# Performance work log

Hardware: AMD Instinct MI355X
Metric: run time of the kernel (lower is better)

## Reference

```python
import jax, jax.numpy as jnp
import numpy as np

N_NODES = 50000
N_EDGES = 800000
IN, HID, OUT = 512, 256, 128


def spmm(edge_src, edge_dst, edge_weight, x, n_nodes):
    # y[i] = sum_{e: dst[e]==i} w[e] * x[src[e]]   (sparse adjacency @ x)
    msgs = edge_weight[:, None] * x[edge_src]          # [E, F] gather
    return jax.ops.segment_sum(msgs, edge_dst, num_segments=n_nodes)


def setup_inputs() -> dict:
    key = jax.random.key(0)
    k1, k2, k3, k4, k5, k6 = jax.random.split(key, 6)
    features = jax.random.normal(k1, (N_NODES, IN), dtype=jnp.float32)
    edge_src = jax.random.randint(k2, (N_EDGES,), 0, N_NODES, dtype=jnp.int32)
    edge_dst = jax.random.randint(k3, (N_EDGES,), 0, N_NODES, dtype=jnp.int32)
    edge_weight = jax.random.uniform(k4, (N_EDGES,), dtype=jnp.float32)
    # init like torch: uniform(-stdv, stdv), stdv = 1/sqrt(out_dim)
    s1 = 1.0 / np.sqrt(HID)
    s2 = 1.0 / np.sqrt(OUT)
    W1 = jax.random.uniform(k5, (IN, HID), dtype=jnp.float32, minval=-s1, maxval=s1)
    W2 = jax.random.uniform(k6, (HID, OUT), dtype=jnp.float32, minval=-s2, maxval=s2)
    return {"features": features, "edge_src": edge_src, "edge_dst": edge_dst,
            "edge_weight": edge_weight, "W1": W1, "W2": W2}


def reference(features, edge_src, edge_dst, edge_weight, W1, W2):
    n = features.shape[0]
    # layer 1: dense GEMM -> SpMM -> ReLU
    hidden = jax.nn.relu(spmm(edge_src, edge_dst, edge_weight, features @ W1, n))
    # layer 2: dense GEMM -> SpMM
    out = spmm(edge_src, edge_dst, edge_weight, hidden @ W2, n)
    return out
```

## Files before the change

kernel.cpp:

```cpp
#include <hip/hip_runtime.h>

#define NN 50000
#define NE 800000
#define FIN 512
#define FHID 256
#define FOUT 128
#define MPAD 50048

#define TW1_BLOCKS  512
#define TW2_BLOCKS  128
#define ZERO_BLOCKS 13

#define NBKT   196
#define BCAP   5120
#define BSTRIDE 16
#define PA_BLOCKS 392
#define E_CHA    2048

#define PB_BLOCKS    196
#define GEMM1_BLOCKS 1564
#define GEMM2_BLOCKS 782

using bf16x8 = __attribute__((ext_vector_type(8))) short;
using f32x4  = __attribute__((ext_vector_type(4))) float;
using u16x8  = __attribute__((ext_vector_type(8))) unsigned short;
using u16x4  = __attribute__((ext_vector_type(4))) unsigned short;

__device__ __forceinline__ unsigned short f2bf(float f) {
    unsigned int u = __builtin_bit_cast(unsigned int, f);
    unsigned int r = (u + 0x7FFFu + ((u >> 16) & 1u)) >> 16;
    return (unsigned short)r;
}
__device__ __forceinline__ float bf2f(unsigned short u) {
    return __builtin_bit_cast(float, (unsigned int)u << 16);
}
__device__ __forceinline__ void gload_lds16(const void* g, void* l) {
    __builtin_amdgcn_global_load_lds(
        (const __attribute__((address_space(1))) void*)g,
        (__attribute__((address_space(3))) void*)l, 16, 0, 0);
}


__global__ __launch_bounds__(256) void prep_kernel(
    int* __restrict__ bcur,
    const float* __restrict__ W1, unsigned short* __restrict__ W1T,
    const float* __restrict__ W2, unsigned short* __restrict__ W2T) {
    int b = blockIdx.x, tid = threadIdx.x;
    if (b < TW1_BLOCKS) {
        int t = b * 256 + tid;
        int n = t % FHID, k = t / FHID;
        W1T[(size_t)n * FIN + k] = f2bf(W1[t]);
    } else if (b < TW1_BLOCKS + TW2_BLOCKS) {
        int t = (b - TW1_BLOCKS) * 256 + tid;
        int n = t % FOUT, k = t / FOUT;
        W2T[(size_t)n * FHID + k] = f2bf(W2[t]);
    } else {
        int i = (b - TW1_BLOCKS - TW2_BLOCKS) * 256 + tid;
        if (i < NBKT * BSTRIDE) bcur[i] = 0;
    }
}


__device__ __forceinline__ void passa_body(int pa,
                                           const int* __restrict__ src,
                                           const int* __restrict__ dst,
                                           const float* __restrict__ w,
                                           int* __restrict__ bcur,
                                           int2* __restrict__ barr) {
    __shared__ int hist[NBKT];
    __shared__ int resv[NBKT];
    int tid = threadIdx.x;
    if (tid < NBKT) hist[tid] = 0;
    __syncthreads();
    int base = pa * E_CHA + tid;
    int  d[8];
    bool m[8];
#pragma unroll
    for (int j = 0; j < 8; ++j) {
        int e = base + j * 256;
        m[j] = e < NE;
        d[j] = m[j] ? dst[e] : 0;
    }
#pragma unroll
    for (int j = 0; j < 8; ++j)
        if (m[j]) atomicAdd(&hist[d[j] >> 8], 1);
    __syncthreads();
    if (tid < NBKT) {
        int h = hist[tid];
        resv[tid] = (h > 0) ? atomicAdd(&bcur[tid * BSTRIDE], h) : 0;
        hist[tid] = 0;
    }
    __syncthreads();
    int   s[8];
    float wv[8];
#pragma unroll
    for (int j = 0; j < 8; ++j) {
        int e = base + j * 256;
        s[j]  = m[j] ? src[e] : 0;
        wv[j] = m[j] ? w[e] : 0.f;
    }
#pragma unroll
    for (int j = 0; j < 8; ++j) {
        if (m[j]) {
            int bb = d[j] >> 8;
            int r  = atomicAdd(&hist[bb], 1);
            int pos = resv[bb] + r;
            if (pos < BCAP)
                barr[(size_t)bb * BCAP + pos] =
                    make_int2(s[j] | ((d[j] & 255) << 16), __float_as_int(wv[j]));
        }
    }
}


__device__ __forceinline__ void gemm1_body(const float* __restrict__ X,
                                           const unsigned short* __restrict__ BT,
                                           unsigned short* __restrict__ C,
                                           int bx, int by) {
    __shared__ unsigned short As[64 * 64];
    __shared__ unsigned short Bs[128 * 64];

    const int tid  = threadIdx.x;
    const int lane = tid & 63;
    const int wid  = tid >> 6;
    const int wm   = wid >> 1;
    const int wn   = wid & 1;
    const int brow = bx * 64;
    const int bcol = by * 128;
    const int r15   = lane & 15;
    const int khalf = (lane >> 4) * 8;

    f32x4 acc[2][4] = {};

    for (int k0 = 0; k0 < FIN; k0 += 64) {
#pragma unroll
        for (int c = 0; c < 4; ++c) {
            int b   = wid * 4096 + c * 1024 + lane * 16;
            int row = b >> 7;
            int cby = (b & 127) ^ ((row & 7) << 4);
            const char* gb = (const char*)(BT + (size_t)(bcol + row) * FIN + k0) + cby;
            gload_lds16(gb, (char*)Bs + wid * 4096 + c * 1024);
        }
#pragma unroll
        for (int g = 0; g < 2; ++g) {
            int idx  = g * 256 + tid;
            int row  = idx >> 3;
            int col0 = (idx & 7) * 8;
            float4 a0 = make_float4(0.f, 0.f, 0.f, 0.f), a1 = a0;
            int grow = brow + row;
            if (grow < NN) {
                const float4* p = (const float4*)(X + (size_t)grow * FIN + k0 + col0);
                a0 = p[0]; a1 = p[1];
            }
            u16x8 v;
            v[0] = f2bf(a0.x); v[1] = f2bf(a0.y); v[2] = f2bf(a0.z); v[3] = f2bf(a0.w);
            v[4] = f2bf(a1.x); v[5] = f2bf(a1.y); v[6] = f2bf(a1.z); v[7] = f2bf(a1.w);
            int byte = row * 128 + ((col0 * 2) ^ ((row & 7) << 4));
            *(u16x8*)((char*)As + byte) = v;
        }
        __syncthreads();

        bf16x8 af[2][2], bfr[4][2];
#pragma unroll
        for (int m = 0; m < 2; ++m) {
            int row = wm * 32 + m * 16 + r15;
            int rb  = row * 128;
            int sw  = (row & 7) << 4;
#pragma unroll
            for (int ks = 0; ks < 2; ++ks) {
                int byte = rb + (((ks * 32 + khalf) * 2) ^ sw);
                af[m][ks] = *(const bf16x8*)((const char*)As + byte);
            }
        }
#pragma unroll
        for (int n = 0; n < 4; ++n) {
            int row = wn * 64 + n * 16 + r15;
            int rb  = row * 128;
            int sw  = (row & 7) << 4;
#pragma unroll
            for (int ks = 0; ks < 2; ++ks) {
                int byte = rb + (((ks * 32 + khalf) * 2) ^ sw);
                bfr[n][ks] = *(const bf16x8*)((const char*)Bs + byte);
            }
        }
#pragma unroll
        for (int m = 0; m < 2; ++m)
#pragma unroll
            for (int n = 0; n < 4; ++n)
#pragma unroll
                for (int ks = 0; ks < 2; ++ks)
                    acc[m][n] = __builtin_amdgcn_mfma_f32_16x16x32_bf16(
                        af[m][ks], bfr[n][ks], acc[m][n], 0, 0, 0);
        __syncthreads();
    }

    const int crow0 = brow + wm * 32;
    const int ccol0 = bcol + wn * 64 + r15;
    const int rsub  = (lane >> 4) * 4;
#pragma unroll
    for (int m = 0; m < 2; ++m) {
#pragma unroll
        for (int r = 0; r < 4; ++r) {
            int grow = crow0 + m * 16 + rsub + r;
            if (grow < NN) {
#pragma unroll
                for (int n = 0; n < 4; ++n)
                    C[(size_t)grow * FHID + ccol0 + n * 16] = f2bf(acc[m][n][r]);
            }
        }
    }
}


__global__ __launch_bounds__(256) void fused_passa_gemm1_kernel(
    const int* __restrict__ src, const int* __restrict__ dst,
    const float* __restrict__ w, int* __restrict__ bcur, int2* __restrict__ barr,
    const float* __restrict__ X, const unsigned short* __restrict__ BT,
    unsigned short* __restrict__ C) {
    if (blockIdx.x < PA_BLOCKS) {
        passa_body(blockIdx.x, src, dst, w, bcur, barr);
    } else {
        int g = blockIdx.x - PA_BLOCKS;
        gemm1_body(X, BT, C, g >> 1, g & 1);
    }
}


__global__ __launch_bounds__(256) void passb_kernel(const int2* __restrict__ barr,
                                                    const int* __restrict__ bcur,
                                                    int* __restrict__ off,
                                                    int2* __restrict__ csr) {
    __shared__ int sc[256];
    __shared__ int cnt[256];
    __shared__ int pre[256];
    __shared__ int wsum[4];
    int b = blockIdx.x, tid = threadIdx.x, lane = tid & 63, wid = tid >> 6;

    int v = (tid < NBKT) ? min(bcur[tid * BSTRIDE], BCAP) : 0;
    int s = v;
#pragma unroll
    for (int d = 1; d < 64; d <<= 1) {
        int t = __shfl_up(s, d, 64);
        if (lane >= d) s += t;
    }
    if (lane == 63) wsum[wid] = s;
    __syncthreads();
    int wo = 0;
#pragma unroll
    for (int j = 0; j < 4; ++j)
        if (j < wid) wo += wsum[j];
    sc[tid] = wo + s - v;
    if (b == 0 && tid == NBKT - 1) off[NN] = wo + s;
    cnt[tid] = 0;
    __syncthreads();

    int bko_b = sc[b];
    int total = min(bcur[b * BSTRIDE], BCAP);
    const int2* seg = barr + (size_t)b * BCAP;

    for (int k = tid; k < total; k += 256)
        atomicAdd(&cnt[(seg[k].x >> 16) & 255], 1);
    __syncthreads();
    int v2 = cnt[tid];
    int s2 = v2;
#pragma unroll
    for (int d = 1; d < 64; d <<= 1) {
        int t = __shfl_up(s2, d, 64);
        if (lane >= d) s2 += t;
    }
    if (lane == 63) wsum[wid] = s2;
    __syncthreads();
    int wo2 = 0;
#pragma unroll
    for (int j = 0; j < 4; ++j)
        if (j < wid) wo2 += wsum[j];
    int base = bko_b + wo2 + s2 - v2;
    pre[tid] = base;
    int n = b * 256 + tid;
    if (n < NN) off[n] = base;
    cnt[tid] = 0;
    __syncthreads();
    for (int k = tid; k < total; k += 256) {
        int2 pl = seg[k];
        int dlow = (pl.x >> 16) & 255;
        int r = atomicAdd(&cnt[dlow], 1);
        csr[pre[dlow] + r] = make_int2(pl.x & 0xFFFF, pl.y);
    }
}


__global__ __launch_bounds__(256) void gemm2_kernel(const unsigned short* __restrict__ A,
                                                    const unsigned short* __restrict__ BT,
                                                    unsigned short* __restrict__ C) {
    __shared__ unsigned short As[64 * 64];
    __shared__ unsigned short Bs[128 * 64];

    const int tid  = threadIdx.x;
    const int lane = tid & 63;
    const int wid  = tid >> 6;
    const int wm   = wid >> 1;
    const int wn   = wid & 1;
    const int brow = blockIdx.x * 64;
    const int r15   = lane & 15;
    const int khalf = (lane >> 4) * 8;

    f32x4 acc[2][4] = {};

    for (int k0 = 0; k0 < FHID; k0 += 64) {
#pragma unroll
        for (int c = 0; c < 4; ++c) {
            int b   = wid * 4096 + c * 1024 + lane * 16;
            int row = b >> 7;
            int cby = (b & 127) ^ ((row & 7) << 4);
            const char* gb = (const char*)(BT + (size_t)row * FHID + k0) + cby;
            gload_lds16(gb, (char*)Bs + wid * 4096 + c * 1024);
        }
#pragma unroll
        for (int c = 0; c < 2; ++c) {
            int b   = wid * 2048 + c * 1024 + lane * 16;
            int row = b >> 7;
            int cby = (b & 127) ^ ((row & 7) << 4);
            const char* ga = (const char*)(A + (size_t)(brow + row) * FHID + k0) + cby;
            gload_lds16(ga, (char*)As + wid * 2048 + c * 1024);
        }
        __syncthreads();

        bf16x8 af[2][2], bfr[4][2];
#pragma unroll
        for (int m = 0; m < 2; ++m) {
            int row = wm * 32 + m * 16 + r15;
            int rb  = row * 128;
            int sw  = (row & 7) << 4;
#pragma unroll
            for (int ks = 0; ks < 2; ++ks) {
                int byte = rb + (((ks * 32 + khalf) * 2) ^ sw);
                af[m][ks] = *(const bf16x8*)((const char*)As + byte);
            }
        }
#pragma unroll
        for (int n = 0; n < 4; ++n) {
            int row = wn * 64 + n * 16 + r15;
            int rb  = row * 128;
            int sw  = (row & 7) << 4;
#pragma unroll
            for (int ks = 0; ks < 2; ++ks) {
                int byte = rb + (((ks * 32 + khalf) * 2) ^ sw);
                bfr[n][ks] = *(const bf16x8*)((const char*)Bs + byte);
            }
        }
#pragma unroll
        for (int m = 0; m < 2; ++m)
#pragma unroll
            for (int n = 0; n < 4; ++n)
#pragma unroll
                for (int ks = 0; ks < 2; ++ks)
                    acc[m][n] = __builtin_amdgcn_mfma_f32_16x16x32_bf16(
                        af[m][ks], bfr[n][ks], acc[m][n], 0, 0, 0);
        __syncthreads();
    }

    const int crow0 = brow + wm * 32;
    const int ccol0 = wn * 64 + r15;
    const int rsub  = (lane >> 4) * 4;
#pragma unroll
    for (int m = 0; m < 2; ++m) {
#pragma unroll
        for (int r = 0; r < 4; ++r) {
            int grow = crow0 + m * 16 + rsub + r;
            if (grow < NN) {
#pragma unroll
                for (int n = 0; n < 4; ++n)
                    C[(size_t)grow * FOUT + ccol0 + n * 16] = f2bf(acc[m][n][r]);
            }
        }
    }
}


__global__ __launch_bounds__(256) void spmm_pair_kernel(const unsigned short* __restrict__ X,
                                                        const int* __restrict__ off,
                                                        const int2* __restrict__ csr,
                                                        unsigned short* __restrict__ Y) {
    int wave = (int)((blockIdx.x * 256 + threadIdx.x) >> 6);
    int lane = threadIdx.x & 63;
    int half = lane >> 5;
    int hl   = lane & 31;
    int n = wave * 2 + half;
    if (n >= NN) return;
    int e0 = off[n];
    int e1 = off[n + 1];
    const size_t fo = (size_t)hl * 8;

    float acc[8] = {};
    for (int e = e0; e < e1; e += 8) {
        int   ss[8];
        float ww[8];
#pragma unroll
        for (int j = 0; j < 8; ++j) {
            int  ee = e + j;
            bool v  = ee < e1;
            int2 sw = csr[v ? ee : e0];
            ss[j] = sw.x;
            ww[j] = v ? __int_as_float(sw.y) : 0.f;
        }
        u16x8 r[8];
#pragma unroll
        for (int j = 0; j < 8; ++j)
            r[j] = *(const u16x8*)(X + (size_t)ss[j] * FHID + fo);
#pragma unroll
        for (int j = 0; j < 8; ++j)
#pragma unroll
            for (int k = 0; k < 8; ++k)
                acc[k] += ww[j] * bf2f(r[j][k]);
    }
    u16x8 o;
#pragma unroll
    for (int k = 0; k < 8; ++k) o[k] = f2bf(fmaxf(acc[k], 0.f));
    *(u16x8*)(Y + (size_t)n * FHID + fo) = o;
}


__global__ __launch_bounds__(256) void spmm_quad_kernel(const unsigned short* __restrict__ X,
                                                        const int* __restrict__ off,
                                                        const int2* __restrict__ csr,
                                                        float* __restrict__ Y) {
    int wave = (int)((blockIdx.x * 256 + threadIdx.x) >> 6);
    int lane = threadIdx.x & 63;
    int q  = lane >> 4;
    int hl = lane & 15;
    int n = wave * 4 + q;
    if (n >= NN) return;
    int e0 = off[n];
    int e1 = off[n + 1];
    const size_t fo = (size_t)hl * 8;

    float acc[8] = {};
    for (int e = e0; e < e1; e += 8) {
        int   ss[8];
        float ww[8];
#pragma unroll
        for (int j = 0; j < 8; ++j) {
            int  ee = e + j;
            bool v  = ee < e1;
            int2 sw = csr[v ? ee : e0];
            ss[j] = sw.x;
            ww[j] = v ? __int_as_float(sw.y) : 0.f;
        }
        u16x8 r[8];
#pragma unroll
        for (int j = 0; j < 8; ++j)
            r[j] = *(const u16x8*)(X + (size_t)ss[j] * FOUT + fo);
#pragma unroll
        for (int j = 0; j < 8; ++j)
#pragma unroll
            for (int k = 0; k < 8; ++k)
                acc[k] += ww[j] * bf2f(r[j][k]);
    }
    float4 o0 = make_float4(acc[0], acc[1], acc[2], acc[3]);
    float4 o1 = make_float4(acc[4], acc[5], acc[6], acc[7]);
    *(float4*)(Y + (size_t)n * FOUT + fo) = o0;
    *(float4*)(Y + (size_t)n * FOUT + fo + 4) = o1;
}


extern "C" void kernel_launch(void* const* d_in, const int* in_sizes, int n_in,
                              void* d_out, int out_size, void* d_ws, size_t ws_size,
                              hipStream_t stream) {
    const float* features = (const float*)d_in[0];
    const int*   edge_src = (const int*)d_in[1];
    const int*   edge_dst = (const int*)d_in[2];
    const float* edge_w   = (const float*)d_in[3];
    const float* W1       = (const float*)d_in[4];
    const float* W2       = (const float*)d_in[5];
    float* out = (float*)d_out;

    char*  ws  = (char*)d_ws;
    size_t ofs = 0;
    auto carve = [&](size_t bytes) -> void* {
        void* r = ws + ofs;
        ofs = (ofs + bytes + 255) & ~(size_t)255;
        return r;
    };
    int*            off   = (int*)carve((NN + 1) * sizeof(int));
    int*            bcur  = (int*)carve(NBKT * BSTRIDE * sizeof(int));
    int2*           barr  = (int2*)carve((size_t)NBKT * BCAP * sizeof(int2));
    int2*           csr   = (int2*)carve((size_t)NE * sizeof(int2));
    unsigned short* W1T   = (unsigned short*)carve((size_t)FHID * FIN * 2);
    unsigned short* W2T   = (unsigned short*)carve((size_t)FOUT * FHID * 2);
    unsigned short* H0b   = (unsigned short*)carve((size_t)MPAD * FHID * 2);
    unsigned short* Hb    = (unsigned short*)carve((size_t)MPAD * FHID * 2);
    unsigned short* H1b   = H0b;

    prep_kernel<<<TW1_BLOCKS + TW2_BLOCKS + ZERO_BLOCKS, 256, 0, stream>>>(
        bcur, W1, W1T, W2, W2T);

    fused_passa_gemm1_kernel<<<PA_BLOCKS + GEMM1_BLOCKS, 256, 0, stream>>>(
        edge_src, edge_dst, edge_w, bcur, barr, features, W1T, H0b);

    passb_kernel<<<PB_BLOCKS, 256, 0, stream>>>(barr, bcur, off, csr);

    spmm_pair_kernel<<<6250, 256, 0, stream>>>(H0b, off, csr, Hb);

    gemm2_kernel<<<GEMM2_BLOCKS, 256, 0, stream>>>(Hb, W2T, H1b);
    spmm_quad_kernel<<<3125, 256, 0, stream>>>(H1b, off, csr, out);
}
```

Baseline: 168.2 us.

## Double-buffer LDS tiles in both GEMM kernels to overlap loads with MFMA

Both GEMM kernels now keep two LDS buffers for the A and B tiles. The next K-slice is fetched while MFMAs run on the current one: global_load_lds for B (and A in gemm2), and register prefetch plus a deferred bf16 convert-and-store for A in gemm1. This drops one barrier per iteration and hides global load latency behind compute. In exchange, LDS use per block doubles to 48KB, which may lower occupancy, and gemm1 keeps extra prefetch registers live.

Measured after the change: 169.5 us. No clear change (+0.8%).

```diff
diff --git a/kernel.cpp b/kernel.cpp
--- a/kernel.cpp
+++ b/kernel.cpp
@@ -24,7 +24,6 @@
 using bf16x8 = __attribute__((ext_vector_type(8))) short;
 using f32x4  = __attribute__((ext_vector_type(4))) float;
 using u16x8  = __attribute__((ext_vector_type(8))) unsigned short;
-using u16x4  = __attribute__((ext_vector_type(4))) unsigned short;
 
 __device__ __forceinline__ unsigned short f2bf(float f) {
     unsigned int u = __builtin_bit_cast(unsigned int, f);
@@ -117,8 +116,8 @@
                                            const unsigned short* __restrict__ BT,
                                            unsigned short* __restrict__ C,
                                            int bx, int by) {
-    __shared__ unsigned short As[64 * 64];
-    __shared__ unsigned short Bs[128 * 64];
+    __shared__ unsigned short As[2][64 * 64];
+    __shared__ unsigned short Bs[2][128 * 64];
 
     const int tid  = threadIdx.x;
     const int lane = tid & 63;
@@ -130,36 +129,58 @@
     const int r15   = lane & 15;
     const int khalf = (lane >> 4) * 8;
 
+    const int arow0 = tid >> 3;
+    const int arow1 = (256 + tid) >> 3;
+    const int acol  = (tid & 7) * 8;
+    const bool aok0 = (brow + arow0) < NN;
+    const bool aok1 = (brow + arow1) < NN;
+    const float4* ap0 = (const float4*)(X + (size_t)(brow + arow0) * FIN + acol);
+    const float4* ap1 = (const float4*)(X + (size_t)(brow + arow1) * FIN + acol);
+    const int abyte0 = arow0 * 128 + ((acol * 2) ^ ((arow0 & 7) << 4));
+    const int abyte1 = arow1 * 128 + ((acol * 2) ^ ((arow1 & 7) << 4));
+
     f32x4 acc[2][4] = {};
-
-    for (int k0 = 0; k0 < FIN; k0 += 64) {
+    float4 a00, a01, a10, a11;
+
+    auto issueB = [&](int k0, int buf) {
 #pragma unroll
         for (int c = 0; c < 4; ++c) {
             int b   = wid * 4096 + c * 1024 + lane * 16;
             int row = b >> 7;
             int cby = (b & 127) ^ ((row & 7) << 4);
             const char* gb = (const char*)(BT + (size_t)(bcol + row) * FIN + k0) + cby;
-            gload_lds16(gb, (char*)Bs + wid * 4096 + c * 1024);
-        }
-#pragma unroll
-        for (int g = 0; g < 2; ++g) {
-            int idx  = g * 256 + tid;
-            int row  = idx >> 3;
-            int col0 = (idx & 7) * 8;
-            float4 a0 = make_float4(0.f, 0.f, 0.f, 0.f), a1 = a0;
-            int grow = brow + row;
-            if (grow < NN) {
-                const float4* p = (const float4*)(X + (size_t)grow * FIN + k0 + col0);
-                a0 = p[0]; a1 = p[1];
-            }
-            u16x8 v;
-            v[0] = f2bf(a0.x); v[1] = f2bf(a0.y); v[2] = f2bf(a0.z); v[3] = f2bf(a0.w);
-            v[4] = f2bf(a1.x); v[5] = f2bf(a1.y); v[6] = f2bf(a1.z); v[7] = f2bf(a1.w);
-            int byte = row * 128 + ((col0 * 2) ^ ((row & 7) << 4));
-            *(u16x8*)((char*)As + byte) = v;
-        }
-        __syncthreads();
-
+            gload_lds16(gb, (char*)Bs[buf] + wid * 4096 + c * 1024);
+        }
+    };
+    auto loadA = [&](int k0) {
+        float4 z = make_float4(0.f, 0.f, 0.f, 0.f);
+        a00 = z; a01 = z; a10 = z; a11 = z;
+        int q = k0 >> 2;
+        if (aok0) { a00 = ap0[q]; a01 = ap0[q + 1]; }
+        if (aok1) { a10 = ap1[q]; a11 = ap1[q + 1]; }
+    };
+    auto writeA = [&](int buf) {
+        u16x8 v;
+        v[0] = f2bf(a00.x); v[1] = f2bf(a00.y); v[2] = f2bf(a00.z); v[3] = f2bf(a00.w);
+        v[4] = f2bf(a01.x); v[5] = f2bf(a01.y); v[6] = f2bf(a01.z); v[7] = f2bf(a01.w);
+        *(u16x8*)((char*)As[buf] + abyte0) = v;
+        v[0] = f2bf(a10.x); v[1] = f2bf(a10.y); v[2] = f2bf(a10.z); v[3] = f2bf(a10.w);
+        v[4] = f2bf(a11.x); v[5] = f2bf(a11.y); v[6] = f2bf(a11.z); v[7] = f2bf(a11.w);
+        *(u16x8*)((char*)As[buf] + abyte1) = v;
+    };
+
+    issueB(0, 0);
+    loadA(0);
+    writeA(0);
+    __syncthreads();
+
+#pragma unroll
+    for (int k = 0; k < 8; ++k) {
+        const int cur = k & 1, nxt = cur ^ 1;
+        if (k < 7) {
+            issueB((k + 1) * 64, nxt);
+            loadA((k + 1) * 64);
+        }
         bf16x8 af[2][2], bfr[4][2];
 #pragma unroll
         for (int m = 0; m < 2; ++m) {
@@ -169,7 +190,7 @@
 #pragma unroll
             for (int ks = 0; ks < 2; ++ks) {
                 int byte = rb + (((ks * 32 + khalf) * 2) ^ sw);
-                af[m][ks] = *(const bf16x8*)((const char*)As + byte);
+                af[m][ks] = *(const bf16x8*)((const char*)As[cur] + byte);
             }
         }
 #pragma unroll
@@ -180,7 +201,7 @@
 #pragma unroll
             for (int ks = 0; ks < 2; ++ks) {
                 int byte = rb + (((ks * 32 + khalf) * 2) ^ sw);
-                bfr[n][ks] = *(const bf16x8*)((const char*)Bs + byte);
+                bfr[n][ks] = *(const bf16x8*)((const char*)Bs[cur] + byte);
             }
         }
 #pragma unroll
@@ -191,6 +212,7 @@
                 for (int ks = 0; ks < 2; ++ks)
                     acc[m][n] = __builtin_amdgcn_mfma_f32_16x16x32_bf16(
                         af[m][ks], bfr[n][ks], acc[m][n], 0, 0, 0);
+        if (k < 7) writeA(nxt);
         __syncthreads();
     }
 
@@ -292,8 +314,8 @@
 __global__ __launch_bounds__(256) void gemm2_kernel(const unsigned short* __restrict__ A,
                                                     const unsigned short* __restrict__ BT,
                                                     unsigned short* __restrict__ C) {
-    __shared__ unsigned short As[64 * 64];
-    __shared__ unsigned short Bs[128 * 64];
+    __shared__ unsigned short As[2][64 * 64];
+    __shared__ unsigned short Bs[2][128 * 64];
 
     const int tid  = threadIdx.x;
     const int lane = tid & 63;
@@ -306,14 +328,14 @@
 
     f32x4 acc[2][4] = {};
 
-    for (int k0 = 0; k0 < FHID; k0 += 64) {
+    auto stage = [&](int k0, int buf) {
 #pragma unroll
         for (int c = 0; c < 4; ++c) {
             int b   = wid * 4096 + c * 1024 + lane * 16;
             int row = b >> 7;
             int cby = (b & 127) ^ ((row & 7) << 4);
             const char* gb = (const char*)(BT + (size_t)row * FHID + k0) + cby;
-            gload_lds16(gb, (char*)Bs + wid * 4096 + c * 1024);
+            gload_lds16(gb, (char*)Bs[buf] + wid * 4096 + c * 1024);
         }
 #pragma unroll
         for (int c = 0; c < 2; ++c) {
@@ -321,9 +343,17 @@
             int row = b >> 7;
             int cby = (b & 127) ^ ((row & 7) << 4);
             const char* ga = (const char*)(A + (size_t)(brow + row) * FHID + k0) + cby;
-            gload_lds16(ga, (char*)As + wid * 2048 + c * 1024);
-        }
-        __syncthreads();
+            gload_lds16(ga, (char*)As[buf] + wid * 2048 + c * 1024);
+        }
+    };
+
+    stage(0, 0);
+    __syncthreads();
+
+#pragma unroll
+    for (int k = 0; k < 4; ++k) {
+        const int cur = k & 1, nxt = cur ^ 1;
+        if (k < 3) stage((k + 1) * 64, nxt);
 
         bf16x8 af[2][2], bfr[4][2];
 #pragma unroll
@@ -334,7 +364,7 @@
 #pragma unroll
             for (int ks = 0; ks < 2; ++ks) {
                 int byte = rb + (((ks * 32 + khalf) * 2) ^ sw);
-                af[m][ks] = *(const bf16x8*)((const char*)As + byte);
+                af[m][ks] = *(const bf16x8*)((const char*)As[cur] + byte);
             }
         }
 #pragma unroll
@@ -345,7 +375,7 @@
 #pragma unroll
             for (int ks = 0; ks < 2; ++ks) {
                 int byte = rb + (((ks * 32 + khalf) * 2) ^ sw);
-                bfr[n][ks] = *(const bf16x8*)((const char*)Bs + byte);
+                bfr[n][ks] = *(const bf16x8*)((const char*)Bs[cur] + byte);
             }
         }
 #pragma unroll
```

## Widen GEMM tiles to full output width and regroup pass-A with weight prep

Applied to the files above, without the earlier changes.

GEMM1 now computes a full 64x256 output tile per block, so each fp32 feature row is read and converted to bf16 once instead of twice. It also register-prefetches the next A slice while the current one is computed. GEMM2 switches to a 4x2 per-wave layout covering all 128 columns. Edge bucketing (pass A) moves out of the GEMM1 launch and into the weight-transpose prep kernel, and bucket counters are zeroed with a memset. The trade-offs are that pass A no longer overlaps GEMM1, GEMM1 uses more LDS and registers (lower occupancy), and there is one extra launch.

New measurement: 169.5 us. No clear change (+0.8%).

```diff
diff --git a/kernel.cpp b/kernel.cpp
--- a/kernel.cpp
+++ b/kernel.cpp
@@ -9,7 +9,6 @@
 
 #define TW1_BLOCKS  512
 #define TW2_BLOCKS  128
-#define ZERO_BLOCKS 13
 
 #define NBKT   196
 #define BCAP   5120
@@ -17,14 +16,11 @@
 #define PA_BLOCKS 392
 #define E_CHA    2048
 
-#define PB_BLOCKS    196
-#define GEMM1_BLOCKS 1564
-#define GEMM2_BLOCKS 782
+#define PB_BLOCKS 196
 
 using bf16x8 = __attribute__((ext_vector_type(8))) short;
 using f32x4  = __attribute__((ext_vector_type(4))) float;
 using u16x8  = __attribute__((ext_vector_type(8))) unsigned short;
-using u16x4  = __attribute__((ext_vector_type(4))) unsigned short;
 
 __device__ __forceinline__ unsigned short f2bf(float f) {
     unsigned int u = __builtin_bit_cast(unsigned int, f);
@@ -41,187 +37,158 @@
 }
 
 
-__global__ __launch_bounds__(256) void prep_kernel(
-    int* __restrict__ bcur,
+__global__ __launch_bounds__(256) void fused_passa_prep_kernel(
+    const int* __restrict__ src, const int* __restrict__ dst,
+    const float* __restrict__ w, int* __restrict__ bcur, int2* __restrict__ barr,
     const float* __restrict__ W1, unsigned short* __restrict__ W1T,
     const float* __restrict__ W2, unsigned short* __restrict__ W2T) {
     int b = blockIdx.x, tid = threadIdx.x;
-    if (b < TW1_BLOCKS) {
-        int t = b * 256 + tid;
+    if (b < PA_BLOCKS) {
+        __shared__ int hist[NBKT];
+        __shared__ int resv[NBKT];
+        if (tid < NBKT) hist[tid] = 0;
+        __syncthreads();
+        int base = b * E_CHA + tid;
+        int  d[8];
+        bool m[8];
+#pragma unroll
+        for (int j = 0; j < 8; ++j) {
+            int e = base + j * 256;
+            m[j] = e < NE;
+            d[j] = m[j] ? dst[e] : 0;
+        }
+#pragma unroll
+        for (int j = 0; j < 8; ++j)
+            if (m[j]) atomicAdd(&hist[d[j] >> 8], 1);
+        __syncthreads();
+        if (tid < NBKT) {
+            int h = hist[tid];
+            resv[tid] = (h > 0) ? atomicAdd(&bcur[tid * BSTRIDE], h) : 0;
+            hist[tid] = 0;
+        }
+        __syncthreads();
+        int   s[8];
+        float wv[8];
+#pragma unroll
+        for (int j = 0; j < 8; ++j) {
+            int e = base + j * 256;
+            s[j]  = m[j] ? src[e] : 0;
+            wv[j] = m[j] ? w[e] : 0.f;
+        }
+#pragma unroll
+        for (int j = 0; j < 8; ++j) {
+            if (m[j]) {
+                int bb = d[j] >> 8;
+                int r  = atomicAdd(&hist[bb], 1);
+                int pos = resv[bb] + r;
+                if (pos < BCAP)
+                    barr[(size_t)bb * BCAP + pos] =
+                        make_int2(s[j] | ((d[j] & 255) << 16), __float_as_int(wv[j]));
+            }
+        }
+    } else if (b < PA_BLOCKS + TW1_BLOCKS) {
+        int t = (b - PA_BLOCKS) * 256 + tid;
         int n = t % FHID, k = t / FHID;
         W1T[(size_t)n * FIN + k] = f2bf(W1[t]);
-    } else if (b < TW1_BLOCKS + TW2_BLOCKS) {
-        int t = (b - TW1_BLOCKS) * 256 + tid;
+    } else {
+        int t = (b - PA_BLOCKS - TW1_BLOCKS) * 256 + tid;
         int n = t % FOUT, k = t / FOUT;
         W2T[(size_t)n * FHID + k] = f2bf(W2[t]);
-    } else {
-        int i = (b - TW1_BLOCKS - TW2_BLOCKS) * 256 + tid;
-        if (i < NBKT * BSTRIDE) bcur[i] = 0;
-    }
-}
-
-
-__device__ __forceinline__ void passa_body(int pa,
-                                           const int* __restrict__ src,
-                                           const int* __restrict__ dst,
-                                           const float* __restrict__ w,
-                                           int* __restrict__ bcur,
-                                           int2* __restrict__ barr) {
-    __shared__ int hist[NBKT];
-    __shared__ int resv[NBKT];
-    int tid = threadIdx.x;
-    if (tid < NBKT) hist[tid] = 0;
-    __syncthreads();
-    int base = pa * E_CHA + tid;
-    int  d[8];
-    bool m[8];
-#pragma unroll
-    for (int j = 0; j < 8; ++j) {
-        int e = base + j * 256;
-        m[j] = e < NE;
-        d[j] = m[j] ? dst[e] : 0;
-    }
-#pragma unroll
-    for (int j = 0; j < 8; ++j)
-        if (m[j]) atomicAdd(&hist[d[j] >> 8], 1);
-    __syncthreads();
-    if (tid < NBKT) {
-        int h = hist[tid];
-        resv[tid] = (h > 0) ? atomicAdd(&bcur[tid * BSTRIDE], h) : 0;
-        hist[tid] = 0;
-    }
-    __syncthreads();
-    int   s[8];
-    float wv[8];
-#pragma unroll
-    for (int j = 0; j < 8; ++j) {
-        int e = base + j * 256;
-        s[j]  = m[j] ? src[e] : 0;
-        wv[j] = m[j] ? w[e] : 0.f;
-    }
-#pragma unroll
-    for (int j = 0; j < 8; ++j) {
-        if (m[j]) {
-            int bb = d[j] >> 8;
-            int r  = atomicAdd(&hist[bb], 1);
-            int pos = resv[bb] + r;
-            if (pos < BCAP)
-                barr[(size_t)bb * BCAP + pos] =
-                    make_int2(s[j] | ((d[j] & 255) << 16), __float_as_int(wv[j]));
-        }
-    }
-}
-
-
-__device__ __forceinline__ void gemm1_body(const float* __restrict__ X,
-                                           const unsigned short* __restrict__ BT,
-                                           unsigned short* __restrict__ C,
-                                           int bx, int by) {
+    }
+}
+
+
+__global__ __launch_bounds__(256) void gemm1_kernel(const float* __restrict__ X,
+                                                    const unsigned short* __restrict__ BT,
+                                                    unsigned short* __restrict__ C) {
     __shared__ unsigned short As[64 * 64];
-    __shared__ unsigned short Bs[128 * 64];
+    __shared__ unsigned short Bs[256 * 64];
 
     const int tid  = threadIdx.x;
     const int lane = tid & 63;
     const int wid  = tid >> 6;
-    const int wm   = wid >> 1;
-    const int wn   = wid & 1;
-    const int brow = bx * 64;
-    const int bcol = by * 128;
+    const int brow = blockIdx.x * 64;
     const int r15   = lane & 15;
     const int khalf = (lane >> 4) * 8;
 
-    f32x4 acc[2][4] = {};
-
-    for (int k0 = 0; k0 < FIN; k0 += 64) {
-#pragma unroll
-        for (int c = 0; c < 4; ++c) {
-            int b   = wid * 4096 + c * 1024 + lane * 16;
+    const int arow0 = tid >> 3;
+    const int arow1 = 32 + (tid >> 3);
+    const int acol  = (tid & 7) * 8;
+    const int g0 = min(brow + arow0, NN - 1);
+    const int g1 = min(brow + arow1, NN - 1);
+    const float4* ap0 = (const float4*)(X + (size_t)g0 * FIN + acol);
+    const float4* ap1 = (const float4*)(X + (size_t)g1 * FIN + acol);
+    const int ab0 = arow0 * 128 + ((acol * 2) ^ ((arow0 & 7) << 4));
+    const int ab1 = arow1 * 128 + ((acol * 2) ^ ((arow1 & 7) << 4));
+
+    f32x4 acc[4][4] = {};
+    float4 a00 = ap0[0], a01 = ap0[1], a10 = ap1[0], a11 = ap1[1];
+
+#pragma unroll
+    for (int k = 0; k < 8; ++k) {
+        const int k0 = k * 64;
+#pragma unroll
+        for (int c = 0; c < 8; ++c) {
+            int b   = wid * 8192 + c * 1024 + lane * 16;
             int row = b >> 7;
             int cby = (b & 127) ^ ((row & 7) << 4);
-            const char* gb = (const char*)(BT + (size_t)(bcol + row) * FIN + k0) + cby;
-            gload_lds16(gb, (char*)Bs + wid * 4096 + c * 1024);
-        }
-#pragma unroll
-        for (int g = 0; g < 2; ++g) {
-            int idx  = g * 256 + tid;
-            int row  = idx >> 3;
-            int col0 = (idx & 7) * 8;
-            float4 a0 = make_float4(0.f, 0.f, 0.f, 0.f), a1 = a0;
-            int grow = brow + row;
-            if (grow < NN) {
-                const float4* p = (const float4*)(X + (size_t)grow * FIN + k0 + col0);
-                a0 = p[0]; a1 = p[1];
-            }
+            const char* gb = (const char*)(BT + (size_t)row * FIN + k0) + cby;
+            gload_lds16(gb, (char*)Bs + wid * 8192 + c * 1024);
+        }
+        {
             u16x8 v;
-            v[0] = f2bf(a0.x); v[1] = f2bf(a0.y); v[2] = f2bf(a0.z); v[3] = f2bf(a0.w);
-            v[4] = f2bf(a1.x); v[5] = f2bf(a1.y); v[6] = f2bf(a1.z); v[7] = f2bf(a1.w);
-            int byte = row * 128 + ((col0 * 2) ^ ((row & 7) << 4));
-            *(u16x8*)((char*)As + byte) = v;
-        }
-        __syncthreads();
-
-        bf16x8 af[2][2], bfr[4][2];
-#pragma unroll
-        for (int m = 0; m < 2; ++m) {
-            int row = wm * 32 + m * 16 + r15;
+            v[0] = f2bf(a00.x); v[1] = f2bf(a00.y); v[2] = f2bf(a00.z); v[3] = f2bf(a00.w);
+            v[4] = f2bf(a01.x); v[5] = f2bf(a01.y); v[6] = f2bf(a01.z); v[7] = f2bf(a01.w);
+            *(u16x8*)((char*)As + ab0) = v;
+            v[0] = f2bf(a10.x); v[1] = f2bf(a10.y); v[2] = f2bf(a10.z); v[3] = f2bf(a10.w);
+            v[4] = f2bf(a11.x); v[5] = f2bf(a11.y); v[6] = f2bf(a11.z); v[7] = f2bf(a11.w);
+            *(u16x8*)((char*)As + ab1) = v;
+        }
+        __syncthreads();
+
+        if (k < 7) {
+            int q = (k0 + 64) >> 2;
+            a00 = ap0[q]; a01 = ap0[q + 1]; a10 = ap1[q]; a11 = ap1[q + 1];
+        }
+
+        bf16x8 bfr[4][2];
+#pragma unroll
+        for (int n = 0; n < 4; ++n) {
+            int row = wid * 64 + n * 16 + r15;
             int rb  = row * 128;
             int sw  = (row & 7) << 4;
 #pragma unroll
-            for (int ks = 0; ks < 2; ++ks) {
-                int byte = rb + (((ks * 32 + khalf) * 2) ^ sw);
-                af[m][ks] = *(const bf16x8*)((const char*)As + byte);
-            }
-        }
-#pragma unroll
-        for (int n = 0; n < 4; ++n) {
-            int row = wn * 64 + n * 16 + r15;
+            for (int ks = 0; ks < 2; ++ks)
+                bfr[n][ks] = *(const bf16x8*)((const char*)Bs + rb + (((ks * 32 + khalf) * 2) ^ sw));
+        }
+#pragma unroll
+        for (int m = 0; m < 4; ++m) {
+            int row = m * 16 + r15;
             int rb  = row * 128;
             int sw  = (row & 7) << 4;
-#pragma unroll
-            for (int ks = 0; ks < 2; ++ks) {
-                int byte = rb + (((ks * 32 + khalf) * 2) ^ sw);
-                bfr[n][ks] = *(const bf16x8*)((const char*)Bs + byte);
+            bf16x8 af0 = *(const bf16x8*)((const char*)As + rb + (((0 + khalf) * 2) ^ sw));
+            bf16x8 af1 = *(const bf16x8*)((const char*)As + rb + (((32 + khalf) * 2) ^ sw));
+#pragma unroll
+            for (int n = 0; n < 4; ++n) {
+                acc[m][n] = __builtin_amdgcn_mfma_f32_16x16x32_bf16(af0, bfr[n][0], acc[m][n], 0, 0, 0);
+                acc[m][n] = __builtin_amdgcn_mfma_f32_16x16x32_bf16(af1, bfr[n][1], acc[m][n], 0, 0, 0);
             }
         }
-#pragma unroll
-        for (int m = 0; m < 2; ++m)
-#pragma unroll
-            for (int n = 0; n < 4; ++n)
-#pragma unroll
-                for (int ks = 0; ks < 2; ++ks)
-                    acc[m][n] = __builtin_amdgcn_mfma_f32_16x16x32_bf16(
-                        af[m][ks], bfr[n][ks], acc[m][n], 0, 0, 0);
-        __syncthreads();
-    }
-
-    const int crow0 = brow + wm * 32;
-    const int ccol0 = bcol + wn * 64 + r15;
-    const int rsub  = (lane >> 4) * 4;
-#pragma unroll
-    for (int m = 0; m < 2; ++m) {
+        __syncthreads();
+    }
+
+    const int rsub = (lane >> 4) * 4;
+#pragma unroll
+    for (int m = 0; m < 4; ++m) {
 #pragma unroll
         for (int r = 0; r < 4; ++r) {
-            int grow = crow0 + m * 16 + rsub + r;
+            int grow = brow + m * 16 + rsub + r;
             if (grow < NN) {
 #pragma unroll
                 for (int n = 0; n < 4; ++n)
-                    C[(size_t)grow * FHID + ccol0 + n * 16] = f2bf(acc[m][n][r]);
+                    C[(size_t)grow * FHID + wid * 64 + n * 16 + r15] = f2bf(acc[m][n][r]);
             }
         }
-    }
-}
-
-
-__global__ __launch_bounds__(256) void fused_passa_gemm1_kernel(
-    const int* __restrict__ src, const int* __restrict__ dst,
-    const float* __restrict__ w, int* __restrict__ bcur, int2* __restrict__ barr,
-    const float* __restrict__ X, const unsigned short* __restrict__ BT,
-    unsigned short* __restrict__ C) {
-    if (blockIdx.x < PA_BLOCKS) {
-        passa_body(blockIdx.x, src, dst, w, bcur, barr);
-    } else {
-        int g = blockIdx.x - PA_BLOCKS;
-        gemm1_body(X, BT, C, g >> 1, g & 1);
     }
 }
 
@@ -298,15 +265,15 @@
     const int tid  = threadIdx.x;
     const int lane = tid & 63;
     const int wid  = tid >> 6;
-    const int wm   = wid >> 1;
-    const int wn   = wid & 1;
     const int brow = blockIdx.x * 64;
     const int r15   = lane & 15;
     const int khalf = (lane >> 4) * 8;
 
-    f32x4 acc[2][4] = {};
-
-    for (int k0 = 0; k0 < FHID; k0 += 64) {
+    f32x4 acc[4][2] = {};
+
+#pragma unroll
+    for (int k = 0; k < 4; ++k) {
+        const int k0 = k * 64;
 #pragma unroll
         for (int c = 0; c < 4; ++c) {
             int b   = wid * 4096 + c * 1024 + lane * 16;
@@ -325,52 +292,42 @@
         }
         __syncthreads();
 
-        bf16x8 af[2][2], bfr[4][2];
-#pragma unroll
-        for (int m = 0; m < 2; ++m) {
-            int row = wm * 32 + m * 16 + r15;
+        bf16x8 bfr[2][2];
+#pragma unroll
+        for (int n = 0; n < 2; ++n) {
+            int row = wid * 32 + n * 16 + r15;
             int rb  = row * 128;
             int sw  = (row & 7) << 4;
 #pragma unroll
-            for (int ks = 0; ks < 2; ++ks) {
-                int byte = rb + (((ks * 32 + khalf) * 2) ^ sw);
-                af[m][ks] = *(const bf16x8*)((const char*)As + byte);
-            }
-        }
-#pragma unroll
-        for (int n = 0; n < 4; ++n) {
-            int row = wn * 64 + n * 16 + r15;
+            for (int ks = 0; ks < 2; ++ks)
+                bfr[n][ks] = *(const bf16x8*)((const char*)Bs + rb + (((ks * 32 + khalf) * 2) ^ sw));
+        }
+#pragma unroll
+        for (int m = 0; m < 4; ++m) {
+            int row = m * 16 + r15;
             int rb  = row * 128;
             int sw  = (row & 7) << 4;
-#pragma unroll
-            for (int ks = 0; ks < 2; ++ks) {
-                int byte = rb + (((ks * 32 + khalf) * 2) ^ sw);
-                bfr[n][ks] = *(const bf16x8*)((const char*)Bs + byte);
+            bf16x8 af0 = *(const bf16x8*)((const char*)As + rb + (((0 + khalf) * 2) ^ sw));
+            bf16x8 af1 = *(const bf16x8*)((const char*)As + rb + (((32 + khalf) * 2) ^ sw));
+#pragma unroll
+            for (int n = 0; n < 2; ++n) {
+                acc[m][n] = __builtin_amdgcn_mfma_f32_16x16x32_bf16(af0, bfr[n][0], acc[m][n], 0, 0, 0);
+                acc[m][n] = __builtin_amdgcn_mfma_f32_16x16x32_bf16(af1, bfr[n][1], acc[m][n], 0, 0, 0);
             }
         }
-#pragma unroll
-        for (int m = 0; m < 2; ++m)
-#pragma unroll
-            for (int n = 0; n < 4; ++n)
-#pragma unroll
-                for (int ks = 0; ks < 2; ++ks)
-                    acc[m][n] = __builtin_amdgcn_mfma_f32_16x16x32_bf16(
-                        af[m][ks], bfr[n][ks], acc[m][n], 0, 0, 0);
-        __syncthreads();
-    }
-
-    const int crow0 = brow + wm * 32;
-    const int ccol0 = wn * 64 + r15;
-    const int rsub  = (lane >> 4) * 4;
-#pragma unroll
-    for (int m = 0; m < 2; ++m) {
+        __syncthreads();
+    }
+
+    const int rsub = (lane >> 4) * 4;
+#pragma unroll
+    for (int m = 0; m < 4; ++m) {
 #pragma unroll
         for (int r = 0; r < 4; ++r) {
-            int grow = crow0 + m * 16 + rsub + r;
+            int grow = brow + m * 16 + rsub + r;
             if (grow < NN) {
 #pragma unroll
-                for (int n = 0; n < 4; ++n)
-                    C[(size_t)grow * FOUT + ccol0 + n * 16] = f2bf(acc[m][n][r]);
+                for (int n = 0; n < 2; ++n)
+                    C[(size_t)grow * FOUT + wid * 32 + n * 16 + r15] = f2bf(acc[m][n][r]);
             }
         }
     }
@@ -491,16 +448,17 @@
     unsigned short* Hb    = (unsigned short*)carve((size_t)MPAD * FHID * 2);
     unsigned short* H1b   = H0b;
 
-    prep_kernel<<<TW1_BLOCKS + TW2_BLOCKS + ZERO_BLOCKS, 256, 0, stream>>>(
-        bcur, W1, W1T, W2, W2T);
-
-    fused_passa_gemm1_kernel<<<PA_BLOCKS + GEMM1_BLOCKS, 256, 0, stream>>>(
-        edge_src, edge_dst, edge_w, bcur, barr, features, W1T, H0b);
+    hipMemsetAsync(bcur, 0, NBKT * BSTRIDE * sizeof(int), stream);
+
+    fused_passa_prep_kernel<<<PA_BLOCKS + TW1_BLOCKS + TW2_BLOCKS, 256, 0, stream>>>(
+        edge_src, edge_dst, edge_w, bcur, barr, W1, W1T, W2, W2T);
+
+    gemm1_kernel<<<MPAD / 64, 256, 0, stream>>>(features, W1T, H0b);
 
     passb_kernel<<<PB_BLOCKS, 256, 0, stream>>>(barr, bcur, off, csr);
 
     spmm_pair_kernel<<<6250, 256, 0, stream>>>(H0b, off, csr, Hb);
 
-    gemm2_kernel<<<GEMM2_BLOCKS, 256, 0, stream>>>(Hb, W2T, H1b);
+    gemm2_kernel<<<MPAD / 64, 256, 0, stream>>>(Hb, W2T, H1b);
     spmm_quad_kernel<<<3125, 256, 0, stream>>>(H1b, off, csr, out);
 }
```
